# Performance work log

Hardware: AMD Instinct MI355X
Metric: run time of the kernel (lower is better)

Reference implementation:

```python
import jax, jax.numpy as jnp
import numpy as np

RES = 16          # grid resolution per axis -> num_models = 4096
L_XYZ = 10        # xyz positional-encoding frequencies -> input_ch = 63
L_DIR = 4         # dir positional-encoding frequencies -> input_ch_views = 27
W = 32
N_RAYS, N_SAMPLES = 1024, 128
NM = RES * RES * RES


def _embed(x, L):
    # NeRF frequency encoding: [x, sin(2^k x), cos(2^k x)] for k in 0..L-1
    freqs = 2.0 ** jnp.arange(L, dtype=x.dtype)          # (L,)
    xf = x[..., None, :] * freqs[:, None]                # (N, L, 3)
    enc = jnp.concatenate([jnp.sin(xf), jnp.cos(xf)], axis=-1)
    return jnp.concatenate([x, enc.reshape(x.shape[0], -1)], axis=-1)


def setup_inputs() -> dict:
    key = jax.random.key(0)
    ks = jax.random.split(key, 16)
    s = 0.05
    pts = jax.random.uniform(ks[0], (N_RAYS, N_SAMPLES, 3), dtype=jnp.float32)
    vd = jax.random.normal(ks[1], (N_RAYS, 3), dtype=jnp.float32)
    vd = vd / jnp.linalg.norm(vd, axis=-1, keepdims=True)
    return {
        "pts": pts,
        "viewdirs": vd,
        "pts_w0": s * jax.random.normal(ks[2], (NM, W, 63), dtype=jnp.float32),
        "pts_b0": s * jax.random.normal(ks[3], (NM, W), dtype=jnp.float32),
        "pts_w1": s * jax.random.normal(ks[4], (NM, W, W), dtype=jnp.float32),
        "pts_b1": s * jax.random.normal(ks[5], (NM, W), dtype=jnp.float32),
        "feat_w": s * jax.random.normal(ks[6], (NM, W, W), dtype=jnp.float32),
        "feat_b": s * jax.random.normal(ks[7], (NM, W), dtype=jnp.float32),
        "sigma_w": s * jax.random.normal(ks[8], (NM, 1, W), dtype=jnp.float32),
        "sigma_b": s * jax.random.normal(ks[9], (NM, 1), dtype=jnp.float32),
        "view_w": s * jax.random.normal(ks[10], (NM, W, W + 27), dtype=jnp.float32),
        "view_b": s * jax.random.normal(ks[11], (NM, W), dtype=jnp.float32),
        "rgb_w": s * jax.random.normal(ks[12], (NM, 3, W), dtype=jnp.float32),
        "rgb_b": s * jax.random.normal(ks[13], (NM, 3), dtype=jnp.float32),
    }


def reference(pts, viewdirs, pts_w0, pts_b0, pts_w1, pts_b1, feat_w, feat_b,
              sigma_w, sigma_b, view_w, view_b, rgb_w, rgb_b):
    n_rays, n_samples, _ = pts.shape
    p = pts.reshape(-1, 3)                                        # (N, 3)
    v = jnp.broadcast_to(viewdirs[:, None, :],
                         (n_rays, n_samples, 3)).reshape(-1, 3)   # (N, 3)

    # voxel index (aabb = [0,1]^3)
    scaled = jnp.clip(p * RES, 0.0, RES - 1.0)
    i3 = scaled.astype(jnp.int32)
    idx = i3[:, 0] * (RES * RES) + i3[:, 1] * RES + i3[:, 2]      # (N,)

    ep = _embed(p, L_XYZ)                                         # (N, 63)
    ev = _embed(v, L_DIR)                                         # (N, 27)

    # per-point tiny MLP with gathered weights: h @ w^T + b
    h = jax.nn.relu(jnp.einsum('nd,nod->no', ep, pts_w0[idx]) + pts_b0[idx])
    h = jax.nn.relu(jnp.einsum('nd,nod->no', h, pts_w1[idx]) + pts_b1[idx])

    sigma = jnp.einsum('nd,nod->no', h, sigma_w[idx]) + sigma_b[idx]   # (N, 1)
    feat = jnp.einsum('nd,nod->no', h, feat_w[idx]) + feat_b[idx]      # (N, W)

    h2 = jnp.concatenate([feat, ev], axis=-1)                          # (N, W+27)
    h2 = jax.nn.relu(jnp.einsum('nd,nod->no', h2, view_w[idx]) + view_b[idx])
    rgb = jnp.einsum('nd,nod->no', h2, rgb_w[idx]) + rgb_b[idx]        # (N, 3)

    out = jnp.concatenate([rgb, sigma], axis=-1).reshape(n_rays, n_samples, 4)
    return out[..., :3], out[..., 3:4]
```

## Files before the change

kernel.cpp:

```cpp
#include <hip/hip_runtime.h>

#define NM    4096
#define NPTS  131072
#define CAP   128

typedef _Float16 h8 __attribute__((ext_vector_type(8)));
typedef _Float16 h2 __attribute__((ext_vector_type(2)));
typedef float    f4 __attribute__((ext_vector_type(4)));
typedef int      i4 __attribute__((ext_vector_type(4)));

#define MF(a, b, c) __builtin_amdgcn_mfma_f32_16x16x32_f16((a), (b), (c), 0, 0, 0)

#if __has_builtin(__builtin_amdgcn_global_load_lds)
#define USE_DMA 1
#else
#define USE_DMA 0
#endif

static __device__ inline h2 pk(float a, float b) {
    return __builtin_bit_cast(h2, __builtin_amdgcn_cvt_pkrtz(a, b));
}

static __device__ inline h8 pack8(float u0, float u1, float u2, float u3,
                                  float u4, float u5, float u6, float u7) {
    i4 t;
    t[0] = __builtin_bit_cast(int, pk(u0, u1));
    t[1] = __builtin_bit_cast(int, pk(u2, u3));
    t[2] = __builtin_bit_cast(int, pk(u4, u5));
    t[3] = __builtin_bit_cast(int, pk(u6, u7));
    return __builtin_bit_cast(h8, t);
}

static __device__ inline h8 lds_row8(const float* __restrict__ X, int base,
                                     int d0, int lim) {
    float u[8];
    #pragma unroll
    for (int jj = 0; jj < 8; jj++) {
        int d = d0 + jj;
        float raw = X[base + d];
        u[jj] = (d < lim) ? raw : 0.f;
    }
    return pack8(u[0], u[1], u[2], u[3], u[4], u[5], u[6], u[7]);
}

static __device__ inline h8 lds_row8a(const float* __restrict__ X, int off) {
    f4 v0 = *(const f4*)(X + off);
    f4 v1 = *(const f4*)(X + off + 4);
    return pack8(v0[0], v0[1], v0[2], v0[3], v1[0], v1[1], v1[2], v1[3]);
}

static __device__ inline h8 load_row8(const float* __restrict__ rb, int d0, int lim) {
    float u[8];
    #pragma unroll
    for (int jj = 0; jj < 8; jj++) {
        int d = d0 + jj;
        u[jj] = (d < lim) ? rb[d] : 0.f;
    }
    return pack8(u[0], u[1], u[2], u[3], u[4], u[5], u[6], u[7]);
}

static __device__ inline float encdim(int d, int lim, float x, float y, float z) {
    int tt = d - 3;
    int k  = tt / 6;
    int r  = tt - 6 * k;
    float p = x;
    p = (r == 1 || r == 4) ? y : p;
    p = (r == 2 || r == 5) ? z : p;
    float f   = __int_as_float((k + 127) << 23);
    float arg = p * f + ((r >= 3) ? 1.57079632679f : 0.f);
    float sv  = __sinf(arg);
    float raw = (d == 0) ? x : ((d == 1) ? y : z);
    float val = (d < 3) ? raw : sv;
    return (d < lim) ? val : 0.f;
}

static __device__ inline h8 makeB(f4 d0, f4 d1, int quad, int col) {
    int laneA = ((quad & 1) * 2) * 16 + col;
    int laneB = laneA + 16;
    float a0 = __shfl(d0[0], laneA), b0 = __shfl(d1[0], laneA);
    float a1 = __shfl(d0[1], laneA), b1 = __shfl(d1[1], laneA);
    float a2 = __shfl(d0[2], laneA), b2 = __shfl(d1[2], laneA);
    float a3 = __shfl(d0[3], laneA), b3 = __shfl(d1[3], laneA);
    float a4 = __shfl(d0[0], laneB), b4 = __shfl(d1[0], laneB);
    float a5 = __shfl(d0[1], laneB), b5 = __shfl(d1[1], laneB);
    float a6 = __shfl(d0[2], laneB), b6 = __shfl(d1[2], laneB);
    float a7 = __shfl(d0[3], laneB), b7 = __shfl(d1[3], laneB);
    bool hi = quad >= 2;
    return pack8(hi ? b0 : a0, hi ? b1 : a1, hi ? b2 : a2, hi ? b3 : a3,
                 hi ? b4 : a4, hi ? b5 : a5, hi ? b6 : a6, hi ? b7 : a7);
}

static __device__ inline f4 relu4(f4 a) {
    f4 r;
    r[0] = fmaxf(a[0], 0.f); r[1] = fmaxf(a[1], 0.f);
    r[2] = fmaxf(a[2], 0.f); r[3] = fmaxf(a[3], 0.f);
    return r;
}

#if USE_DMA
static __device__ inline void dma16(const float* g, const float* l) {
    __builtin_amdgcn_global_load_lds(
        (const __attribute__((address_space(1))) void*)g,
        (__attribute__((address_space(3))) void*)l, 16, 0, 0);
}
#endif

__global__ __launch_bounds__(256) void k_bucket(const float* __restrict__ pts,
                                                int* __restrict__ count,
                                                int* __restrict__ plist) {
    int n = blockIdx.x * 256 + threadIdx.x;
    if (n >= NPTS) return;
    float x = pts[3 * n + 0], y = pts[3 * n + 1], z = pts[3 * n + 2];
    int ix = (int)fminf(fmaxf(x * 16.f, 0.f), 15.f);
    int iy = (int)fminf(fmaxf(y * 16.f, 0.f), 15.f);
    int iz = (int)fminf(fmaxf(z * 16.f, 0.f), 15.f);
    int v = (ix << 8) | (iy << 4) | iz;
    int pos = atomicAdd(&count[v], 1);
    if (pos < CAP) plist[v * CAP + pos] = n;
}

__global__ __launch_bounds__(256) void k_mlp(
    const float* __restrict__ pts, const float* __restrict__ vds,
    const float* __restrict__ w0g, const float* __restrict__ b0g,
    const float* __restrict__ w1g, const float* __restrict__ b1g,
    const float* __restrict__ fwg, const float* __restrict__ fbg,
    const float* __restrict__ swg, const float* __restrict__ sbg,
    const float* __restrict__ vwg, const float* __restrict__ vbg,
    const float* __restrict__ rwg, const float* __restrict__ rbg,
    const int* __restrict__ count, const int* __restrict__ plist,
    float* __restrict__ out) {
    __shared__ __align__(16) float X[6080];

    const int v = blockIdx.x;
    const int t = threadIdx.x;
    const int c = min(count[v], CAP);
    if (c == 0) return;

    const int wid  = t >> 6;
    const int lane = t & 63;
    const int col  = lane & 15;
    const int quad = lane >> 4;
    const int k8   = quad * 8;

#if USE_DMA
    if (wid == 0) {
        const float* g = w0g + (size_t)v * 2016;
        #pragma unroll
        for (int k = 0; k < 7; k++) dma16(g + k * 256 + lane * 4, X + k * 256);
        if (lane < 56) dma16(g + 1792 + lane * 4, X + 1792);
    } else if (wid == 1) {
        const float* g = vwg + (size_t)v * 1888;
        #pragma unroll
        for (int k = 0; k < 7; k++) dma16(g + k * 256 + lane * 4, X + 3040 + k * 256);
        if (lane < 24) dma16(g + 1792 + lane * 4, X + 4832);
    } else if (wid == 2) {
        const float* g = w1g + (size_t)v * 1024;
        #pragma unroll
        for (int k = 0; k < 4; k++) dma16(g + k * 256 + lane * 4, X + 2016 + k * 256);
        if (lane < 8)  dma16(swg + (size_t)v * 32 + lane * 4, X + 5952);
        if (lane < 24) dma16(rwg + (size_t)v * 96 + lane * 4, X + 5984);
    } else {
        const float* g = fwg + (size_t)v * 1024;
        #pragma unroll
        for (int k = 0; k < 4; k++) dma16(g + k * 256 + lane * 4, X + 4928 + k * 256);
    }
#endif

    const bool hasWork = (wid * 16) < c;

    float pxc, pyc, pzc, dxc, dyc, dzc;
    int ncur = 0;
    f4 cB0[2], cB1[2], cFB[2], cVB[2];
    float rb0 = 0.f, rb1 = 0.f, rb2 = 0.f, sb = 0.f;
    if (hasWork) {
        int sl = min(wid * 16 + col, c - 1);
        ncur = plist[v * CAP + sl];
        pxc = pts[3 * ncur]; pyc = pts[3 * ncur + 1]; pzc = pts[3 * ncur + 2];
        int ray = ncur >> 7;
        dxc = vds[3 * ray]; dyc = vds[3 * ray + 1]; dzc = vds[3 * ray + 2];
        #pragma unroll
        for (int Ti = 0; Ti < 2; Ti++) {
            #pragma unroll
            for (int r = 0; r < 4; r++) {
                int row = Ti * 16 + quad * 4 + r;
                cB0[Ti][r] = b0g[v * 32 + row];
                cB1[Ti][r] = b1g[v * 32 + row];
                cFB[Ti][r] = fbg[v * 32 + row];
                cVB[Ti][r] = vbg[v * 32 + row];
            }
        }
        rb0 = rbg[v * 3 + 0]; rb1 = rbg[v * 3 + 1]; rb2 = rbg[v * 3 + 2];
        sb  = sbg[v];
    }

#if USE_DMA
    __syncthreads();
#endif
    if (!hasWork) return;

    h8 aW0[2][2], aVW[2][2], aW1[2], aFW[2], aSG, aRGB;
#if USE_DMA
    #pragma unroll
    for (int Ti = 0; Ti < 2; Ti++) {
        int r0 = (Ti * 16 + col) * 63;
        aW0[Ti][0] = lds_row8(X, r0, k8, 63);
        aW0[Ti][1] = lds_row8(X, r0, 32 + k8, 63);
        aW1[Ti] = lds_row8a(X, 2016 + (Ti * 16 + col) * 32 + k8);
        int r1 = 3040 + (Ti * 16 + col) * 59;
        aVW[Ti][0] = lds_row8(X, r1, k8, 59);
        aVW[Ti][1] = lds_row8(X, r1, 32 + k8, 59);
        aFW[Ti] = lds_row8a(X, 4928 + (Ti * 16 + col) * 32 + k8);
    }
    aSG  = (col == 0) ? lds_row8a(X, 5952 + k8) : h8{};
    aRGB = (col < 3) ? lds_row8a(X, 5984 + col * 32 + k8) : h8{};
#else
    #pragma unroll
    for (int Ti = 0; Ti < 2; Ti++) {
        const float* rb = w0g + (size_t)v * 2016 + (Ti * 16 + col) * 63;
        aW0[Ti][0] = load_row8(rb, k8, 63);
        aW0[Ti][1] = load_row8(rb, 32 + k8, 63);
        rb = vwg + (size_t)v * 1888 + (Ti * 16 + col) * 59;
        aVW[Ti][0] = load_row8(rb, k8, 59);
        aVW[Ti][1] = load_row8(rb, 32 + k8, 59);
        aW1[Ti] = load_row8(w1g + (size_t)v * 1024 + (Ti * 16 + col) * 32, k8, 32);
        aFW[Ti] = load_row8(fwg + (size_t)v * 1024 + (Ti * 16 + col) * 32, k8, 32);
    }
    aSG  = (col == 0) ? load_row8(swg + (size_t)v * 32, k8, 32) : h8{};
    aRGB = (col < 3) ? load_row8(rwg + (size_t)v * 96 + col * 32, k8, 32) : h8{};
#endif

    const f4 z4 = {0.f, 0.f, 0.f, 0.f};

    for (int base = wid * 16; base < c; base += 64) {
        const bool active = (base + col) < c;
        const int n = ncur;
        const float px = pxc, py = pyc, pz = pzc;
        const float dx = dxc, dy = dyc, dz = dzc;

        if (base + 64 < c) {
            int sl = min(base + 64 + col, c - 1);
            ncur = plist[v * CAP + sl];
            pxc = pts[3 * ncur]; pyc = pts[3 * ncur + 1]; pzc = pts[3 * ncur + 2];
            int ray = ncur >> 7;
            dxc = vds[3 * ray]; dyc = vds[3 * ray + 1]; dzc = vds[3 * ray + 2];
        }

        h8 bE0 = pack8(encdim(k8 + 0, 63, px, py, pz), encdim(k8 + 1, 63, px, py, pz),
                       encdim(k8 + 2, 63, px, py, pz), encdim(k8 + 3, 63, px, py, pz),
                       encdim(k8 + 4, 63, px, py, pz), encdim(k8 + 5, 63, px, py, pz),
                       encdim(k8 + 6, 63, px, py, pz), encdim(k8 + 7, 63, px, py, pz));
        h8 bE1 = pack8(encdim(32 + k8 + 0, 63, px, py, pz), encdim(32 + k8 + 1, 63, px, py, pz),
                       encdim(32 + k8 + 2, 63, px, py, pz), encdim(32 + k8 + 3, 63, px, py, pz),
                       encdim(32 + k8 + 4, 63, px, py, pz), encdim(32 + k8 + 5, 63, px, py, pz),
                       encdim(32 + k8 + 6, 63, px, py, pz), encdim(32 + k8 + 7, 63, px, py, pz));

        f4 d0 = MF(aW0[0][0], bE0, cB0[0]); d0 = MF(aW0[0][1], bE1, d0);
        f4 d1 = MF(aW0[1][0], bE0, cB0[1]); d1 = MF(aW0[1][1], bE1, d1);
        d0 = relu4(d0); d1 = relu4(d1);
        h8 bH = makeB(d0, d1, quad, col);

        f4 e0 = MF(aW1[0], bH, cB1[0]);
        f4 e1 = MF(aW1[1], bH, cB1[1]);
        e0 = relu4(e0); e1 = relu4(e1);
        h8 bG = makeB(e0, e1, quad, col);

        f4 s = MF(aSG, bG, z4);

        f4 f0 = MF(aFW[0], bG, cFB[0]);
        f4 f1 = MF(aFW[1], bG, cFB[1]);
        h8 bF = makeB(f0, f1, quad, col);

        h8 bD = pack8(encdim(k8 + 0, 27, dx, dy, dz), encdim(k8 + 1, 27, dx, dy, dz),
                      encdim(k8 + 2, 27, dx, dy, dz), encdim(k8 + 3, 27, dx, dy, dz),
                      encdim(k8 + 4, 27, dx, dy, dz), encdim(k8 + 5, 27, dx, dy, dz),
                      encdim(k8 + 6, 27, dx, dy, dz), encdim(k8 + 7, 27, dx, dy, dz));

        f4 v0 = MF(aVW[0][0], bF, cVB[0]); v0 = MF(aVW[0][1], bD, v0);
        f4 v1 = MF(aVW[1][0], bF, cVB[1]); v1 = MF(aVW[1][1], bD, v1);
        v0 = relu4(v0); v1 = relu4(v1);
        h8 bV = makeB(v0, v1, quad, col);

        f4 o = MF(aRGB, bV, z4);

        if (quad == 0 && active) {
            out[3 * n + 0] = o[0] + rb0;
            out[3 * n + 1] = o[1] + rb1;
            out[3 * n + 2] = o[2] + rb2;
            out[3 * NPTS + n] = s[0] + sb;
        }
    }
}

extern "C" void kernel_launch(void* const* d_in, const int* in_sizes, int n_in,
                              void* d_out, int out_size, void* d_ws, size_t ws_size,
                              hipStream_t stream) {
    const float* pts = (const float*)d_in[0];
    const float* vds = (const float*)d_in[1];
    const float* w0  = (const float*)d_in[2];
    const float* b0  = (const float*)d_in[3];
    const float* w1  = (const float*)d_in[4];
    const float* b1  = (const float*)d_in[5];
    const float* fw  = (const float*)d_in[6];
    const float* fb  = (const float*)d_in[7];
    const float* sw  = (const float*)d_in[8];
    const float* sb  = (const float*)d_in[9];
    const float* vw  = (const float*)d_in[10];
    const float* vb  = (const float*)d_in[11];
    const float* rw  = (const float*)d_in[12];
    const float* rb  = (const float*)d_in[13];
    float* out = (float*)d_out;

    int* count = (int*)d_ws;
    int* plist = (int*)((char*)d_ws + NM * sizeof(int));

    (void)hipMemsetAsync(count, 0, NM * sizeof(int), stream);
    k_bucket<<<NPTS / 256, 256, 0, stream>>>(pts, count, plist);
    k_mlp<<<NM, 256, 0, stream>>>(pts, vds, w0, b0, w1, b1, fw, fb, sw, sb,
                                  vw, vb, rw, rb, count, plist, out);
}
```

Baseline: 176.9 us.

## Process four voxels per block with double-buffered register-staged weight prefetch

Each block now handles four consecutive voxels instead of one. The next voxel's weights are prefetched into registers and then written to a double-buffered LDS region, so the global weight loads overlap with MFMA compute on the current voxel. The async global_load_lds DMA path is replaced by a plain register-staged copy. This cuts the grid size and the per-block setup cost, but it adds register pressure (8 f4 staging registers), doubles LDS use, and serialises four voxels inside one block, which may reduce parallelism across CUs.

```diff
diff --git a/kernel.cpp b/kernel.cpp
--- a/kernel.cpp
+++ b/kernel.cpp
@@ -3,6 +3,8 @@
 #define NM    4096
 #define NPTS  131072
 #define CAP   128
+#define NV    4
+#define NBLK  (NM / NV)
 
 typedef _Float16 h8 __attribute__((ext_vector_type(8)));
 typedef _Float16 h2 __attribute__((ext_vector_type(2)));
@@ -10,12 +12,6 @@
 typedef int      i4 __attribute__((ext_vector_type(4)));
 
 #define MF(a, b, c) __builtin_amdgcn_mfma_f32_16x16x32_f16((a), (b), (c), 0, 0, 0)
-
-#if __has_builtin(__builtin_amdgcn_global_load_lds)
-#define USE_DMA 1
-#else
-#define USE_DMA 0
-#endif
 
 static __device__ inline h2 pk(float a, float b) {
     return __builtin_bit_cast(h2, __builtin_amdgcn_cvt_pkrtz(a, b));
@@ -47,16 +43,6 @@
     f4 v0 = *(const f4*)(X + off);
     f4 v1 = *(const f4*)(X + off + 4);
     return pack8(v0[0], v0[1], v0[2], v0[3], v1[0], v1[1], v1[2], v1[3]);
-}
-
-static __device__ inline h8 load_row8(const float* __restrict__ rb, int d0, int lim) {
-    float u[8];
-    #pragma unroll
-    for (int jj = 0; jj < 8; jj++) {
-        int d = d0 + jj;
-        u[jj] = (d < lim) ? rb[d] : 0.f;
-    }
-    return pack8(u[0], u[1], u[2], u[3], u[4], u[5], u[6], u[7]);
 }
 
 static __device__ inline float encdim(int d, int lim, float x, float y, float z) {
@@ -97,14 +83,6 @@
     return r;
 }
 
-#if USE_DMA
-static __device__ inline void dma16(const float* g, const float* l) {
-    __builtin_amdgcn_global_load_lds(
-        (const __attribute__((address_space(1))) void*)g,
-        (__attribute__((address_space(3))) void*)l, 16, 0, 0);
-}
-#endif
-
 __global__ __launch_bounds__(256) void k_bucket(const float* __restrict__ pts,
                                                 int* __restrict__ count,
                                                 int* __restrict__ plist) {
@@ -129,164 +107,204 @@
     const float* __restrict__ rwg, const float* __restrict__ rbg,
     const int* __restrict__ count, const int* __restrict__ plist,
     float* __restrict__ out) {
-    __shared__ __align__(16) float X[6080];
-
-    const int v = blockIdx.x;
-    const int t = threadIdx.x;
-    const int c = min(count[v], CAP);
-    if (c == 0) return;
-
+    __shared__ __align__(16) float X[2][6080];
+
+    const int bid  = blockIdx.x;
+    const int t    = threadIdx.x;
     const int wid  = t >> 6;
     const int lane = t & 63;
     const int col  = lane & 15;
     const int quad = lane >> 4;
     const int k8   = quad * 8;
-
-#if USE_DMA
-    if (wid == 0) {
-        const float* g = w0g + (size_t)v * 2016;
-        #pragma unroll
-        for (int k = 0; k < 7; k++) dma16(g + k * 256 + lane * 4, X + k * 256);
-        if (lane < 56) dma16(g + 1792 + lane * 4, X + 1792);
-    } else if (wid == 1) {
-        const float* g = vwg + (size_t)v * 1888;
-        #pragma unroll
-        for (int k = 0; k < 7; k++) dma16(g + k * 256 + lane * 4, X + 3040 + k * 256);
-        if (lane < 24) dma16(g + 1792 + lane * 4, X + 4832);
-    } else if (wid == 2) {
-        const float* g = w1g + (size_t)v * 1024;
-        #pragma unroll
-        for (int k = 0; k < 4; k++) dma16(g + k * 256 + lane * 4, X + 2016 + k * 256);
-        if (lane < 8)  dma16(swg + (size_t)v * 32 + lane * 4, X + 5952);
-        if (lane < 24) dma16(rwg + (size_t)v * 96 + lane * 4, X + 5984);
-    } else {
-        const float* g = fwg + (size_t)v * 1024;
-        #pragma unroll
-        for (int k = 0; k < 4; k++) dma16(g + k * 256 + lane * 4, X + 4928 + k * 256);
-    }
-#endif
-
-    const bool hasWork = (wid * 16) < c;
-
-    float pxc, pyc, pzc, dxc, dyc, dzc;
-    int ncur = 0;
-    f4 cB0[2], cB1[2], cFB[2], cVB[2];
-    float rb0 = 0.f, rb1 = 0.f, rb2 = 0.f, sb = 0.f;
-    if (hasWork) {
-        int sl = min(wid * 16 + col, c - 1);
-        ncur = plist[v * CAP + sl];
-        pxc = pts[3 * ncur]; pyc = pts[3 * ncur + 1]; pzc = pts[3 * ncur + 2];
-        int ray = ncur >> 7;
-        dxc = vds[3 * ray]; dyc = vds[3 * ray + 1]; dzc = vds[3 * ray + 2];
-        #pragma unroll
-        for (int Ti = 0; Ti < 2; Ti++) {
-            #pragma unroll
-            for (int r = 0; r < 4; r++) {
-                int row = Ti * 16 + quad * 4 + r;
-                cB0[Ti][r] = b0g[v * 32 + row];
-                cB1[Ti][r] = b1g[v * 32 + row];
-                cFB[Ti][r] = fbg[v * 32 + row];
-                cVB[Ti][r] = vbg[v * 32 + row];
+    const int vbase = bid * NV;
+
+    int cs[NV];
+    #pragma unroll
+    for (int iv = 0; iv < NV; iv++) cs[iv] = min(count[vbase + iv], CAP);
+
+    f4 sreg[8];
+
+    auto stage_issue = [&](int v) {
+        if (wid == 0) {
+            const float* g = w0g + (size_t)v * 2016;
+            #pragma unroll
+            for (int k = 0; k < 7; k++) sreg[k] = *(const f4*)(g + k * 256 + lane * 4);
+            sreg[7] = (lane < 56) ? *(const f4*)(g + 1792 + lane * 4) : f4{0.f, 0.f, 0.f, 0.f};
+        } else if (wid == 1) {
+            const float* g = vwg + (size_t)v * 1888;
+            #pragma unroll
+            for (int k = 0; k < 7; k++) sreg[k] = *(const f4*)(g + k * 256 + lane * 4);
+            sreg[7] = (lane < 24) ? *(const f4*)(g + 1792 + lane * 4) : f4{0.f, 0.f, 0.f, 0.f};
+        } else if (wid == 2) {
+            const float* g = w1g + (size_t)v * 1024;
+            #pragma unroll
+            for (int k = 0; k < 4; k++) sreg[k] = *(const f4*)(g + k * 256 + lane * 4);
+            sreg[4] = (lane < 8)  ? *(const f4*)(swg + (size_t)v * 32 + lane * 4) : f4{0.f, 0.f, 0.f, 0.f};
+            sreg[5] = (lane < 24) ? *(const f4*)(rwg + (size_t)v * 96 + lane * 4) : f4{0.f, 0.f, 0.f, 0.f};
+        } else {
+            const float* g = fwg + (size_t)v * 1024;
+            #pragma unroll
+            for (int k = 0; k < 4; k++) sreg[k] = *(const f4*)(g + k * 256 + lane * 4);
+        }
+    };
+
+    auto stage_write = [&](float* Xb) {
+        if (wid == 0) {
+            #pragma unroll
+            for (int k = 0; k < 7; k++) *(f4*)(Xb + k * 256 + lane * 4) = sreg[k];
+            if (lane < 56) *(f4*)(Xb + 1792 + lane * 4) = sreg[7];
+        } else if (wid == 1) {
+            #pragma unroll
+            for (int k = 0; k < 7; k++) *(f4*)(Xb + 3040 + k * 256 + lane * 4) = sreg[k];
+            if (lane < 24) *(f4*)(Xb + 4832 + lane * 4) = sreg[7];
+        } else if (wid == 2) {
+            #pragma unroll
+            for (int k = 0; k < 4; k++) *(f4*)(Xb + 2016 + k * 256 + lane * 4) = sreg[k];
+            if (lane < 8)  *(f4*)(Xb + 5952 + lane * 4) = sreg[4];
+            if (lane < 24) *(f4*)(Xb + 5984 + lane * 4) = sreg[5];
+        } else {
+            #pragma unroll
+            for (int k = 0; k < 4; k++) *(f4*)(Xb + 4928 + k * 256 + lane * 4) = sreg[k];
+        }
+    };
+
+    int   nn = 0;
+    float npx = 0.f, npy = 0.f, npz = 0.f, ndx = 0.f, ndy = 0.f, ndz = 0.f;
+    auto nextptA = [&](int iv) {
+        int c = cs[iv];
+        if (wid * 16 < c) {
+            int sl = min(wid * 16 + col, c - 1);
+            nn = plist[(vbase + iv) * CAP + sl];
+        }
+    };
+    auto nextptB = [&](int iv) {
+        int c = cs[iv];
+        if (wid * 16 < c) {
+            npx = pts[3 * nn]; npy = pts[3 * nn + 1]; npz = pts[3 * nn + 2];
+            int ray = nn >> 7;
+            ndx = vds[3 * ray]; ndy = vds[3 * ray + 1]; ndz = vds[3 * ray + 2];
+        }
+    };
+
+    stage_issue(vbase);
+    nextptA(0);
+    nextptB(0);
+
+    const f4 z4 = {0.f, 0.f, 0.f, 0.f};
+
+    for (int iv = 0; iv < NV; iv++) {
+        float* Xb = X[iv & 1];
+        stage_write(Xb);
+        __syncthreads();
+
+        int ncur = nn;
+        float pxc = npx, pyc = npy, pzc = npz;
+        float dxc = ndx, dyc = ndy, dzc = ndz;
+
+        if (iv + 1 < NV) {
+            stage_issue(vbase + iv + 1);
+            nextptA(iv + 1);
+        }
+
+        const int c = cs[iv];
+        const bool hasWork = (wid * 16) < c;
+
+        if (hasWork) {
+            f4 cB0[2], cB1[2], cFB[2], cVB[2];
+            #pragma unroll
+            for (int Ti = 0; Ti < 2; Ti++) {
+                #pragma unroll
+                for (int r = 0; r < 4; r++) {
+                    int row = Ti * 16 + quad * 4 + r;
+                    int vv = vbase + iv;
+                    cB0[Ti][r] = b0g[vv * 32 + row];
+                    cB1[Ti][r] = b1g[vv * 32 + row];
+                    cFB[Ti][r] = fbg[vv * 32 + row];
+                    cVB[Ti][r] = vbg[vv * 32 + row];
+                }
             }
-        }
-        rb0 = rbg[v * 3 + 0]; rb1 = rbg[v * 3 + 1]; rb2 = rbg[v * 3 + 2];
-        sb  = sbg[v];
-    }
-
-#if USE_DMA
-    __syncthreads();
-#endif
-    if (!hasWork) return;
-
-    h8 aW0[2][2], aVW[2][2], aW1[2], aFW[2], aSG, aRGB;
-#if USE_DMA
-    #pragma unroll
-    for (int Ti = 0; Ti < 2; Ti++) {
-        int r0 = (Ti * 16 + col) * 63;
-        aW0[Ti][0] = lds_row8(X, r0, k8, 63);
-        aW0[Ti][1] = lds_row8(X, r0, 32 + k8, 63);
-        aW1[Ti] = lds_row8a(X, 2016 + (Ti * 16 + col) * 32 + k8);
-        int r1 = 3040 + (Ti * 16 + col) * 59;
-        aVW[Ti][0] = lds_row8(X, r1, k8, 59);
-        aVW[Ti][1] = lds_row8(X, r1, 32 + k8, 59);
-        aFW[Ti] = lds_row8a(X, 4928 + (Ti * 16 + col) * 32 + k8);
-    }
-    aSG  = (col == 0) ? lds_row8a(X, 5952 + k8) : h8{};
-    aRGB = (col < 3) ? lds_row8a(X, 5984 + col * 32 + k8) : h8{};
-#else
-    #pragma unroll
-    for (int Ti = 0; Ti < 2; Ti++) {
-        const float* rb = w0g + (size_t)v * 2016 + (Ti * 16 + col) * 63;
-        aW0[Ti][0] = load_row8(rb, k8, 63);
-        aW0[Ti][1] = load_row8(rb, 32 + k8, 63);
-        rb = vwg + (size_t)v * 1888 + (Ti * 16 + col) * 59;
-        aVW[Ti][0] = load_row8(rb, k8, 59);
-        aVW[Ti][1] = load_row8(rb, 32 + k8, 59);
-        aW1[Ti] = load_row8(w1g + (size_t)v * 1024 + (Ti * 16 + col) * 32, k8, 32);
-        aFW[Ti] = load_row8(fwg + (size_t)v * 1024 + (Ti * 16 + col) * 32, k8, 32);
-    }
-    aSG  = (col == 0) ? load_row8(swg + (size_t)v * 32, k8, 32) : h8{};
-    aRGB = (col < 3) ? load_row8(rwg + (size_t)v * 96 + col * 32, k8, 32) : h8{};
-#endif
-
-    const f4 z4 = {0.f, 0.f, 0.f, 0.f};
-
-    for (int base = wid * 16; base < c; base += 64) {
-        const bool active = (base + col) < c;
-        const int n = ncur;
-        const float px = pxc, py = pyc, pz = pzc;
-        const float dx = dxc, dy = dyc, dz = dzc;
-
-        if (base + 64 < c) {
-            int sl = min(base + 64 + col, c - 1);
-            ncur = plist[v * CAP + sl];
-            pxc = pts[3 * ncur]; pyc = pts[3 * ncur + 1]; pzc = pts[3 * ncur + 2];
-            int ray = ncur >> 7;
-            dxc = vds[3 * ray]; dyc = vds[3 * ray + 1]; dzc = vds[3 * ray + 2];
-        }
-
-        h8 bE0 = pack8(encdim(k8 + 0, 63, px, py, pz), encdim(k8 + 1, 63, px, py, pz),
-                       encdim(k8 + 2, 63, px, py, pz), encdim(k8 + 3, 63, px, py, pz),
-                       encdim(k8 + 4, 63, px, py, pz), encdim(k8 + 5, 63, px, py, pz),
-                       encdim(k8 + 6, 63, px, py, pz), encdim(k8 + 7, 63, px, py, pz));
-        h8 bE1 = pack8(encdim(32 + k8 + 0, 63, px, py, pz), encdim(32 + k8 + 1, 63, px, py, pz),
-                       encdim(32 + k8 + 2, 63, px, py, pz), encdim(32 + k8 + 3, 63, px, py, pz),
-                       encdim(32 + k8 + 4, 63, px, py, pz), encdim(32 + k8 + 5, 63, px, py, pz),
-                       encdim(32 + k8 + 6, 63, px, py, pz), encdim(32 + k8 + 7, 63, px, py, pz));
-
-        f4 d0 = MF(aW0[0][0], bE0, cB0[0]); d0 = MF(aW0[0][1], bE1, d0);
-        f4 d1 = MF(aW0[1][0], bE0, cB0[1]); d1 = MF(aW0[1][1], bE1, d1);
-        d0 = relu4(d0); d1 = relu4(d1);
-        h8 bH = makeB(d0, d1, quad, col);
-
-        f4 e0 = MF(aW1[0], bH, cB1[0]);
-        f4 e1 = MF(aW1[1], bH, cB1[1]);
-        e0 = relu4(e0); e1 = relu4(e1);
-        h8 bG = makeB(e0, e1, quad, col);
-
-        f4 s = MF(aSG, bG, z4);
-
-        f4 f0 = MF(aFW[0], bG, cFB[0]);
-        f4 f1 = MF(aFW[1], bG, cFB[1]);
-        h8 bF = makeB(f0, f1, quad, col);
-
-        h8 bD = pack8(encdim(k8 + 0, 27, dx, dy, dz), encdim(k8 + 1, 27, dx, dy, dz),
-                      encdim(k8 + 2, 27, dx, dy, dz), encdim(k8 + 3, 27, dx, dy, dz),
-                      encdim(k8 + 4, 27, dx, dy, dz), encdim(k8 + 5, 27, dx, dy, dz),
-                      encdim(k8 + 6, 27, dx, dy, dz), encdim(k8 + 7, 27, dx, dy, dz));
-
-        f4 v0 = MF(aVW[0][0], bF, cVB[0]); v0 = MF(aVW[0][1], bD, v0);
-        f4 v1 = MF(aVW[1][0], bF, cVB[1]); v1 = MF(aVW[1][1], bD, v1);
-        v0 = relu4(v0); v1 = relu4(v1);
-        h8 bV = makeB(v0, v1, quad, col);
-
-        f4 o = MF(aRGB, bV, z4);
-
-        if (quad == 0 && active) {
-            out[3 * n + 0] = o[0] + rb0;
-            out[3 * n + 1] = o[1] + rb1;
-            out[3 * n + 2] = o[2] + rb2;
-            out[3 * NPTS + n] = s[0] + sb;
+            const float rb0 = rbg[(vbase + iv) * 3 + 0];
+            const float rb1 = rbg[(vbase + iv) * 3 + 1];
+            const float rb2 = rbg[(vbase + iv) * 3 + 2];
+            const float sb  = sbg[vbase + iv];
+
+            h8 aW0[2][2], aVW[2][2], aW1[2], aFW[2], aSG, aRGB;
+            #pragma unroll
+            for (int Ti = 0; Ti < 2; Ti++) {
+                int r0 = (Ti * 16 + col) * 63;
+                aW0[Ti][0] = lds_row8(Xb, r0, k8, 63);
+                aW0[Ti][1] = lds_row8(Xb, r0, 32 + k8, 63);
+                aW1[Ti] = lds_row8a(Xb, 2016 + (Ti * 16 + col) * 32 + k8);
+                int r1 = 3040 + (Ti * 16 + col) * 59;
+                aVW[Ti][0] = lds_row8(Xb, r1, k8, 59);
+                aVW[Ti][1] = lds_row8(Xb, r1, 32 + k8, 59);
+                aFW[Ti] = lds_row8a(Xb, 4928 + (Ti * 16 + col) * 32 + k8);
+            }
+            aSG  = (col == 0) ? lds_row8a(Xb, 5952 + k8) : h8{};
+            aRGB = (col < 3) ? lds_row8a(Xb, 5984 + col * 32 + k8) : h8{};
+
+            if (iv + 1 < NV) nextptB(iv + 1);
+
+            for (int base = wid * 16; base < c; base += 64) {
+                const bool active = (base + col) < c;
+                const int n = ncur;
+                const float px = pxc, py = pyc, pz = pzc;
+                const float dx = dxc, dy = dyc, dz = dzc;
+
+                if (base + 64 < c) {
+                    int sl = min(base + 64 + col, c - 1);
+                    ncur = plist[(vbase + iv) * CAP + sl];
+                    pxc = pts[3 * ncur]; pyc = pts[3 * ncur + 1]; pzc = pts[3 * ncur + 2];
+                    int ray = ncur >> 7;
+                    dxc = vds[3 * ray]; dyc = vds[3 * ray + 1]; dzc = vds[3 * ray + 2];
+                }
+
+                h8 bE0 = pack8(encdim(k8 + 0, 63, px, py, pz), encdim(k8 + 1, 63, px, py, pz),
+                               encdim(k8 + 2, 63, px, py, pz), encdim(k8 + 3, 63, px, py, pz),
+                               encdim(k8 + 4, 63, px, py, pz), encdim(k8 + 5, 63, px, py, pz),
+                               encdim(k8 + 6, 63, px, py, pz), encdim(k8 + 7, 63, px, py, pz));
+                h8 bE1 = pack8(encdim(32 + k8 + 0, 63, px, py, pz), encdim(32 + k8 + 1, 63, px, py, pz),
+                               encdim(32 + k8 + 2, 63, px, py, pz), encdim(32 + k8 + 3, 63, px, py, pz),
+                               encdim(32 + k8 + 4, 63, px, py, pz), encdim(32 + k8 + 5, 63, px, py, pz),
+                               encdim(32 + k8 + 6, 63, px, py, pz), encdim(32 + k8 + 7, 63, px, py, pz));
+
+                f4 d0 = MF(aW0[0][0], bE0, cB0[0]); d0 = MF(aW0[0][1], bE1, d0);
+                f4 d1 = MF(aW0[1][0], bE0, cB0[1]); d1 = MF(aW0[1][1], bE1, d1);
+                d0 = relu4(d0); d1 = relu4(d1);
+                h8 bH = makeB(d0, d1, quad, col);
+
+                f4 e0 = MF(aW1[0], bH, cB1[0]);
+                f4 e1 = MF(aW1[1], bH, cB1[1]);
+                e0 = relu4(e0); e1 = relu4(e1);
+                h8 bG = makeB(e0, e1, quad, col);
+
+                f4 s = MF(aSG, bG, z4);
+
+                f4 f0 = MF(aFW[0], bG, cFB[0]);
+                f4 f1 = MF(aFW[1], bG, cFB[1]);
+                h8 bF = makeB(f0, f1, quad, col);
+
+                h8 bD = pack8(encdim(k8 + 0, 27, dx, dy, dz), encdim(k8 + 1, 27, dx, dy, dz),
+                              encdim(k8 + 2, 27, dx, dy, dz), encdim(k8 + 3, 27, dx, dy, dz),
+                              encdim(k8 + 4, 27, dx, dy, dz), encdim(k8 + 5, 27, dx, dy, dz),
+                              encdim(k8 + 6, 27, dx, dy, dz), encdim(k8 + 7, 27, dx, dy, dz));
+
+                f4 v0 = MF(aVW[0][0], bF, cVB[0]); v0 = MF(aVW[0][1], bD, v0);
+                f4 v1 = MF(aVW[1][0], bF, cVB[1]); v1 = MF(aVW[1][1], bD, v1);
+                v0 = relu4(v0); v1 = relu4(v1);
+                h8 bV = makeB(v0, v1, quad, col);
+
+                f4 o = MF(aRGB, bV, z4);
+
+                if (quad == 0 && active) {
+                    out[3 * n + 0] = o[0] + rb0;
+                    out[3 * n + 1] = o[1] + rb1;
+                    out[3 * n + 2] = o[2] + rb2;
+                    out[3 * NPTS + n] = s[0] + sb;
+                }
+            }
+        } else {
+            if (iv + 1 < NV) nextptB(iv + 1);
         }
     }
 }
@@ -315,6 +333,6 @@
 
     (void)hipMemsetAsync(count, 0, NM * sizeof(int), stream);
     k_bucket<<<NPTS / 256, 256, 0, stream>>>(pts, count, plist);
-    k_mlp<<<NM, 256, 0, stream>>>(pts, vds, w0, b0, w1, b1, fw, fb, sw, sb,
-                                  vw, vb, rw, rb, count, plist, out);
-}
+    k_mlp<<<NBLK, 256, 0, stream>>>(pts, vds, w0, b0, w1, b1, fw, fb, sw, sb,
+                                    vw, vb, rw, rb, count, plist, out);
+}
```

After: 209.8 us. +18.6%, slower.
